# Kernel optimization log

Measured on AMD Instinct MI355X. Metric: run time of the kernel, lower is better.

## Reference

```python
import jax, jax.numpy as jnp
import numpy as np
import itertools

N_OBJECTS = 6  # subsets of range(6), sizes 1..6 -> 63 subsets

def _subset_groups():
    # group subsets by length so each group runs as one batched LSTM
    groups = {}
    for m in range(1, N_OBJECTS + 1):
        for s in itertools.combinations(range(6), m):
            groups.setdefault(m, []).append(list(s))
    return [(m, np.asarray(v, dtype=np.int32)) for m, v in groups.items()]

SUBSET_GROUPS = _subset_groups()


def _lstm_final_h(x, W_ih, W_hh, b_ih, b_hh):
    """x: [B,T,D] -> final hidden state [B,H]. PyTorch gate order i,f,g,o."""
    H = W_hh.shape[1]
    B = x.shape[0]
    # precompute input projections for all timesteps: [B,T,4H]
    xz = jnp.einsum('btd,gd->btg', x, W_ih) + b_ih + b_hh

    def step(carry, xt):
        h, c = carry
        z = xt + h @ W_hh.T
        i, f, g, o = jnp.split(z, 4, axis=-1)
        c = jax.nn.sigmoid(f) * c + jax.nn.sigmoid(i) * jnp.tanh(g)
        h = jax.nn.sigmoid(o) * jnp.tanh(c)
        return (h, c), None

    h0 = jnp.zeros((B, H), x.dtype)
    (h, _), _ = jax.lax.scan(step, (h0, h0), jnp.swapaxes(xz, 0, 1))
    return h


def setup_inputs() -> dict:
    key = jax.random.key(0)
    ks = jax.random.split(key, 10)
    D, H, FC, A = 16, 128, 256, 10
    mb = 8192
    s = lambda k, shape, fan: jax.random.normal(k, shape, jnp.float32) * (1.0 / np.sqrt(fan))
    return {
        'x_input': jax.random.normal(ks[0], (mb, 6, D), jnp.float32),
        'W_ih': s(ks[1], (4 * H, D), D),
        'W_hh': s(ks[2], (4 * H, H), H),
        'b_ih': jnp.zeros((4 * H,), jnp.float32),
        'b_hh': jnp.zeros((4 * H,), jnp.float32),
        'fc1_W': s(ks[3], (FC, H), H),
        'fc1_b': jnp.zeros((FC,), jnp.float32),
        'fc2_W': s(ks[4], (A, FC), FC),
        'fc2_b': jnp.zeros((A,), jnp.float32),
    }


def reference(x_input, W_ih, W_hh, b_ih, b_hh, fc1_W, fc1_b, fc2_W, fc2_b):
    mb = x_input.shape[0]
    H = W_hh.shape[1]
    hs = []
    # subsets of the same length are batched into one LSTM pass (fused form of
    # the original 63-iteration python loop); aggregation is permutation-invariant
    for m, idx in SUBSET_GROUPS:
        nL = idx.shape[0]
        xg = x_input[:, idx, :]                       # [mb, nL, m, D] gather
        xg = xg.reshape(mb * nL, m, x_input.shape[-1])
        h = _lstm_final_h(xg, W_ih, W_hh, b_ih, b_hh)  # [mb*nL, H]
        hs.append(h.reshape(mb, nL, H))
    holder = jnp.concatenate(hs, axis=1)              # [mb, 63, H]
    x = jnp.max(holder, axis=1)                       # aggregate == 'max'
    x = jax.nn.relu(x @ fc1_W.T + fc1_b)
    x = x @ fc2_W.T + fc2_b
    return jax.nn.log_softmax(x, axis=-1)
```

## Files before the change

### kernel.cpp

```cpp
#include <hip/hip_runtime.h>
#include <hip/hip_bf16.h>

#define BLOCK   512
#define NSAMP   16
#define HDIM    128
#define DDIM    16
#define NOBJ    6
#define NNODES  63

typedef __attribute__((ext_vector_type(8))) short bf16x8;
typedef __attribute__((ext_vector_type(4))) float f32x4;

struct Tab { int obj[NNODES]; int depth[NNODES]; };
constexpr void tab_dfs(Tab& t, int& n, int maxel, int depth) {
    for (int j = maxel + 1; j < NOBJ; ++j) {
        t.obj[n] = j; t.depth[n] = depth; ++n;
        tab_dfs(t, n, j, depth + 1);
    }
}
constexpr Tab make_tab() { Tab t{}; int n = 0; tab_dfs(t, n, -1, 1); return t; }
constexpr Tab TAB = make_tab();

#define LOG2E  1.44269504f
#define TWOL2E 2.88539008f

__device__ __forceinline__ float fast_sig(float z, float nb) {
    float e = __builtin_amdgcn_exp2f(fmaf(-LOG2E, z, nb));
    return __builtin_amdgcn_rcpf(1.0f + e);
}
__device__ __forceinline__ float fast_tanh_b(float z, float tb) {
    float e = __builtin_amdgcn_exp2f(fmaf(TWOL2E, z, tb));
    float r = __builtin_amdgcn_rcpf(1.0f + e);
    return fmaf(-2.0f, r, 1.0f);
}
__device__ __forceinline__ float fast_tanh(float y) {
    float e = __builtin_amdgcn_exp2f(y * TWOL2E);
    float r = __builtin_amdgcn_rcpf(1.0f + e);
    return fmaf(-2.0f, r, 1.0f);
}
__device__ __forceinline__ unsigned short f2bf(float x) {
    union { float f; unsigned int u; } a; a.f = x;
    unsigned int r = (a.u + 0x7FFFu + ((a.u >> 16) & 1u)) >> 16;
    return (unsigned short)r;
}


__global__ __launch_bounds__(BLOCK, 2)
void subset_lstm_mfma_kernel(
    const float* __restrict__ x_input,
    const float* __restrict__ W_ih,
    const float* __restrict__ W_hh,
    const float* __restrict__ b_ih,
    const float* __restrict__ b_hh,
    const float* __restrict__ fc1_W,
    const float* __restrict__ fc1_b,
    const float* __restrict__ fc2_W,
    const float* __restrict__ fc2_b,
    float* __restrict__ out)
{
    __shared__ __align__(16) unsigned short hs[5 * 16 * NSAMP * 8];
    __shared__ __align__(16) unsigned short xb[NOBJ * 4 * NSAMP * 8];
    __shared__ float s_maxh[NSAMP * HDIM];
    float* s_fc1   = (float*)hs;
    float* s_logit = (float*)xb;

    const int t      = threadIdx.x;
    const int w      = t >> 6;
    const int lane   = t & 63;
    const int quad   = lane >> 4;
    const int m16    = lane & 15;
    const int s_base = blockIdx.x * NSAMP;

    for (int idx = t; idx < NOBJ * 2 * NSAMP * 8; idx += BLOCK) {
        const int j   = idx & 7;
        const int n   = (idx >> 3) & 15;
        const int q   = (idx >> 7) & 1;
        const int obj = idx >> 8;
        xb[((obj * 4 + q) * NSAMP + n) * 8 + j] =
            f2bf(x_input[(s_base + n) * (NOBJ * DDIM) + obj * DDIM + q * 8 + j]);
        xb[((obj * 4 + 2 + q) * NSAMP + n) * 8 + j] = 0;
    }

    bf16x8 wf[4][5];
    #pragma unroll
    for (int g = 0; g < 4; ++g) {
        const int r = g * HDIM + w * 16 + m16;
        const float* whr = W_hh + r * HDIM;
        const float* wir = W_ih + r * DDIM;
        #pragma unroll
        for (int q = 0; q < 4; ++q) {
            union { unsigned short u[8]; bf16x8 v; } pk;
            #pragma unroll
            for (int j = 0; j < 8; ++j)
                pk.u[j] = f2bf(whr[q * 32 + quad * 8 + j]);
            wf[g][q] = pk.v;
        }
        {
            union { unsigned short u[8]; bf16x8 v; } pk;
            #pragma unroll
            for (int j = 0; j < 8; ++j) {
                float v = 0.0f;
                if (quad == 0) v = wir[j];
                else if (quad == 1) v = wir[8 + j];
                pk.u[j] = f2bf(v);
            }
            wf[g][4] = pk.v;
        }
    }

    float bia[4][4];
    #pragma unroll
    for (int g = 0; g < 4; ++g)
        #pragma unroll
        for (int r = 0; r < 4; ++r) {
            const int c = w * 16 + quad * 4 + r;
            const float b = b_ih[g * HDIM + c] + b_hh[g * HDIM + c];
            bia[g][r] = (g == 2) ? TWOL2E * b : -LOG2E * b;
        }

    float cst[5][4];
    float mh[4] = {-1e30f, -1e30f, -1e30f, -1e30f};

    #pragma unroll
    for (int nd = 0; nd < NNODES; ++nd) {
        const int jo = TAB.obj[nd];
        const int d  = TAB.depth[nd];

        __syncthreads();

        f32x4 acc[4];
        #pragma unroll
        for (int g = 0; g < 4; ++g)
            acc[g] = f32x4{0.f, 0.f, 0.f, 0.f};

        if (d >= 2) {
            const int slot = d - 2;
            #pragma unroll
            for (int q = 0; q < 4; ++q) {
                const bf16x8 bfrag = *(const bf16x8*)
                    &hs[(((slot * 16) + q * 4 + quad) * NSAMP + m16) * 8];
                #pragma unroll
                for (int g = 0; g < 4; ++g)
                    acc[g] = __builtin_amdgcn_mfma_f32_16x16x32_bf16(
                        wf[g][q], bfrag, acc[g], 0, 0, 0);
            }
        }
        {
            const bf16x8 bfrag = *(const bf16x8*)
                &xb[((jo * 4 + quad) * NSAMP + m16) * 8];
            #pragma unroll
            for (int g = 0; g < 4; ++g)
                acc[g] = __builtin_amdgcn_mfma_f32_16x16x32_bf16(
                    wf[g][4], bfrag, acc[g], 0, 0, 0);
        }

        float hn[4];
        #pragma unroll
        for (int r = 0; r < 4; ++r) {
            const float cprev = (d >= 2) ? cst[d - 2][r] : 0.0f;
            const float ig = fast_sig(acc[0][r], bia[0][r]);
            const float fg = fast_sig(acc[1][r], bia[1][r]);
            const float gg = fast_tanh_b(acc[2][r], bia[2][r]);
            const float og = fast_sig(acc[3][r], bia[3][r]);
            const float cn = fmaf(fg, cprev, ig * gg);
            const float h  = og * fast_tanh(cn);
            hn[r] = h;
            mh[r] = fmaxf(mh[r], h);
            if (jo < NOBJ - 1) cst[d - 1][r] = cn;
        }

        if (jo < NOBJ - 1) {
            union { __hip_bfloat162 h2[2]; uint2 v; } hp;
            hp.h2[0] = __float22bfloat162_rn(float2{hn[0], hn[1]});
            hp.h2[1] = __float22bfloat162_rn(float2{hn[2], hn[3]});
            const int kslot = w * 2 + (quad >> 1);
            unsigned short* dst =
                &hs[((((d - 1) * 16) + kslot) * NSAMP + m16) * 8 + (quad & 1) * 4];
            *(uint2*)dst = hp.v;
        }
    }

    __syncthreads();
    #pragma unroll
    for (int r = 0; r < 4; ++r) {
        const int c = w * 16 + quad * 4 + r;
        s_maxh[m16 * HDIM + c] = mh[r];
    }
    __syncthreads();

    {
        const int f  = t & 255;
        const int sh = t >> 8;
        float a1[8];
        #pragma unroll
        for (int s = 0; s < 8; ++s) a1[s] = fc1_b[f];
        for (int k4 = 0; k4 < HDIM / 4; ++k4) {
            const float4 wv = *(const float4*)&fc1_W[f * HDIM + k4 * 4];
            #pragma unroll
            for (int s = 0; s < 8; ++s) {
                const float4 h4 = *(const float4*)&s_maxh[(sh * 8 + s) * HDIM + k4 * 4];
                a1[s] += wv.x * h4.x + wv.y * h4.y + wv.z * h4.z + wv.w * h4.w;
            }
        }
        #pragma unroll
        for (int s = 0; s < 8; ++s)
            s_fc1[(sh * 8 + s) * 256 + f] = fmaxf(a1[s], 0.0f);
    }
    __syncthreads();

    if (t < NSAMP * 10) {
        const int s = t / 10, a = t % 10;
        float acc2 = fc2_b[a];
        for (int f4 = 0; f4 < 256 / 4; ++f4) {
            const float4 wv = *(const float4*)&fc2_W[a * 256 + f4 * 4];
            const float4 v  = *(const float4*)&s_fc1[s * 256 + f4 * 4];
            acc2 += wv.x * v.x + wv.y * v.y + wv.z * v.z + wv.w * v.w;
        }
        s_logit[s * 10 + a] = acc2;
    }
    __syncthreads();

    if (t < NSAMP) {
        float m = -1e30f;
        #pragma unroll
        for (int a = 0; a < 10; ++a) m = fmaxf(m, s_logit[t * 10 + a]);
        float sum = 0.0f;
        #pragma unroll
        for (int a = 0; a < 10; ++a) sum += __expf(s_logit[t * 10 + a] - m);
        const float lse = m + __logf(sum);
        #pragma unroll
        for (int a = 0; a < 10; ++a)
            out[(s_base + t) * 10 + a] = s_logit[t * 10 + a] - lse;
    }
}

extern "C" void kernel_launch(void* const* d_in, const int* in_sizes, int n_in,
                              void* d_out, int out_size, void* d_ws, size_t ws_size,
                              hipStream_t stream)
{
    (void)d_ws; (void)ws_size; (void)n_in; (void)out_size;

    const float* x   = (const float*)d_in[0];
    const float* Wih = (const float*)d_in[1];
    const float* Whh = (const float*)d_in[2];
    const float* bih = (const float*)d_in[3];
    const float* bhh = (const float*)d_in[4];
    const float* f1w = (const float*)d_in[5];
    const float* f1b = (const float*)d_in[6];
    const float* f2w = (const float*)d_in[7];
    const float* f2b = (const float*)d_in[8];

    const int mb = in_sizes[0] / (NOBJ * DDIM);
    dim3 grid(mb / NSAMP), block(BLOCK);
    subset_lstm_mfma_kernel<<<grid, block, 0, stream>>>(
        x, Wih, Whh, bih, bhh, f1w, f1b, f2w, f2b, (float*)d_out);
}
```

Before: 216.4 us.

## Traverse subset tree breadth-first to cut barriers and expose node parallelism

```diff
diff --git a/kernel.cpp b/kernel.cpp
--- a/kernel.cpp
+++ b/kernel.cpp
@@ -6,23 +6,42 @@
 #define HDIM    128
 #define DDIM    16
 #define NOBJ    6
-#define NNODES  63
 
 typedef __attribute__((ext_vector_type(8))) short bf16x8;
 typedef __attribute__((ext_vector_type(4))) float f32x4;
 
-struct Tab { int obj[NNODES]; int depth[NNODES]; };
-constexpr void tab_dfs(Tab& t, int& n, int maxel, int depth) {
-    for (int j = maxel + 1; j < NOBJ; ++j) {
-        t.obj[n] = j; t.depth[n] = depth; ++n;
-        tab_dfs(t, n, j, depth + 1);
-    }
-}
-constexpr Tab make_tab() { Tab t{}; int n = 0; tab_dfs(t, n, -1, 1); return t; }
-constexpr Tab TAB = make_tab();
-
-#define LOG2E  1.44269504f
-#define TWOL2E 2.88539008f
+constexpr int msb6(int m) { int b = -1; for (int i = 0; i < 6; ++i) if (m & (1 << i)) b = i; return b; }
+
+struct BfsTab {
+    int cnt[7];
+    int jo[7][20];
+    int pslot[7][20];
+    int slot[7][20];
+};
+constexpr BfsTab make_bfs() {
+    BfsTab t{};
+    int slotOf[64] = {};
+    for (int d = 1; d <= 6; ++d) {
+        int n = 0, cf = 0;
+        for (int M = 1; M < 64; ++M) {
+            if (__builtin_popcount(M) != d) continue;
+            const int hi = msb6(M);
+            t.jo[d][n] = hi;
+            t.pslot[d][n] = (d == 1) ? -1 : slotOf[M & ~(1 << hi)];
+            if (hi < 5) { t.slot[d][n] = cf; slotOf[M] = cf; ++cf; }
+            else t.slot[d][n] = -1;
+            ++n;
+        }
+        t.cnt[d] = n;
+    }
+    return t;
+}
+constexpr BfsTab BT = make_bfs();
+
+#define LOG2E   1.44269504f
+#define TWOL2E  2.88539008f
+#define SLOT_SZ (16 * NSAMP * 8)
+#define EVEN_OFF (10 * SLOT_SZ)
 
 __device__ __forceinline__ float fast_sig(float z, float nb) {
     float e = __builtin_amdgcn_exp2f(fmaf(-LOG2E, z, nb));
@@ -44,9 +63,8 @@
     return (unsigned short)r;
 }
 
-
 __global__ __launch_bounds__(BLOCK, 2)
-void subset_lstm_mfma_kernel(
+void subset_lstm_bfs_kernel(
     const float* __restrict__ x_input,
     const float* __restrict__ W_ih,
     const float* __restrict__ W_hh,
@@ -58,10 +76,10 @@
     const float* __restrict__ fc2_b,
     float* __restrict__ out)
 {
-    __shared__ __align__(16) unsigned short hs[5 * 16 * NSAMP * 8];
+    __shared__ __align__(16) unsigned short hsbuf[20 * SLOT_SZ];
     __shared__ __align__(16) unsigned short xb[NOBJ * 4 * NSAMP * 8];
-    __shared__ float s_maxh[NSAMP * HDIM];
-    float* s_fc1   = (float*)hs;
+    float* s_maxh  = (float*)(hsbuf + EVEN_OFF);
+    float* s_fc1   = (float*)hsbuf;
     float* s_logit = (float*)xb;
 
     const int t      = threadIdx.x;
@@ -118,65 +136,75 @@
             bia[g][r] = (g == 2) ? TWOL2E * b : -LOG2E * b;
         }
 
-    float cst[5][4];
+    float cA[10][4];
+    float cB[10][4];
     float mh[4] = {-1e30f, -1e30f, -1e30f, -1e30f};
 
     #pragma unroll
-    for (int nd = 0; nd < NNODES; ++nd) {
-        const int jo = TAB.obj[nd];
-        const int d  = TAB.depth[nd];
-
+    for (int d = 1; d <= 6; ++d) {
         __syncthreads();
 
-        f32x4 acc[4];
-        #pragma unroll
-        for (int g = 0; g < 4; ++g)
-            acc[g] = f32x4{0.f, 0.f, 0.f, 0.f};
-
-        if (d >= 2) {
-            const int slot = d - 2;
-            #pragma unroll
-            for (int q = 0; q < 4; ++q) {
+        unsigned short*       curbuf = hsbuf + ((d & 1) ? 0 : EVEN_OFF);
+        const unsigned short* parbuf = hsbuf + (((d - 1) & 1) ? 0 : EVEN_OFF);
+
+        #pragma unroll
+        for (int ni = 0; ni < BT.cnt[d]; ++ni) {
+            const int jo = BT.jo[d][ni];
+            const int ps = BT.pslot[d][ni];
+            const int sl = BT.slot[d][ni];
+
+            f32x4 acc[4];
+            #pragma unroll
+            for (int g = 0; g < 4; ++g)
+                acc[g] = f32x4{0.f, 0.f, 0.f, 0.f};
+
+            if (d >= 2) {
+                #pragma unroll
+                for (int q = 0; q < 4; ++q) {
+                    const bf16x8 bfrag = *(const bf16x8*)
+                        &parbuf[ps * SLOT_SZ + (((q * 4 + quad) * NSAMP) + m16) * 8];
+                    #pragma unroll
+                    for (int g = 0; g < 4; ++g)
+                        acc[g] = __builtin_amdgcn_mfma_f32_16x16x32_bf16(
+                            wf[g][q], bfrag, acc[g], 0, 0, 0);
+                }
+            }
+            {
                 const bf16x8 bfrag = *(const bf16x8*)
-                    &hs[(((slot * 16) + q * 4 + quad) * NSAMP + m16) * 8];
+                    &xb[((jo * 4 + quad) * NSAMP + m16) * 8];
                 #pragma unroll
                 for (int g = 0; g < 4; ++g)
                     acc[g] = __builtin_amdgcn_mfma_f32_16x16x32_bf16(
-                        wf[g][q], bfrag, acc[g], 0, 0, 0);
-            }
-        }
-        {
-            const bf16x8 bfrag = *(const bf16x8*)
-                &xb[((jo * 4 + quad) * NSAMP + m16) * 8];
-            #pragma unroll
-            for (int g = 0; g < 4; ++g)
-                acc[g] = __builtin_amdgcn_mfma_f32_16x16x32_bf16(
-                    wf[g][4], bfrag, acc[g], 0, 0, 0);
-        }
-
-        float hn[4];
-        #pragma unroll
-        for (int r = 0; r < 4; ++r) {
-            const float cprev = (d >= 2) ? cst[d - 2][r] : 0.0f;
-            const float ig = fast_sig(acc[0][r], bia[0][r]);
-            const float fg = fast_sig(acc[1][r], bia[1][r]);
-            const float gg = fast_tanh_b(acc[2][r], bia[2][r]);
-            const float og = fast_sig(acc[3][r], bia[3][r]);
-            const float cn = fmaf(fg, cprev, ig * gg);
-            const float h  = og * fast_tanh(cn);
-            hn[r] = h;
-            mh[r] = fmaxf(mh[r], h);
-            if (jo < NOBJ - 1) cst[d - 1][r] = cn;
-        }
-
-        if (jo < NOBJ - 1) {
-            union { __hip_bfloat162 h2[2]; uint2 v; } hp;
-            hp.h2[0] = __float22bfloat162_rn(float2{hn[0], hn[1]});
-            hp.h2[1] = __float22bfloat162_rn(float2{hn[2], hn[3]});
-            const int kslot = w * 2 + (quad >> 1);
-            unsigned short* dst =
-                &hs[((((d - 1) * 16) + kslot) * NSAMP + m16) * 8 + (quad & 1) * 4];
-            *(uint2*)dst = hp.v;
+                        wf[g][4], bfrag, acc[g], 0, 0, 0);
+            }
+
+            float hn[4];
+            #pragma unroll
+            for (int r = 0; r < 4; ++r) {
+                float cprev = 0.0f;
+                if (d >= 2) cprev = ((d - 1) & 1) ? cA[ps][r] : cB[ps][r];
+                const float ig = fast_sig(acc[0][r], bia[0][r]);
+                const float fg = fast_sig(acc[1][r], bia[1][r]);
+                const float gg = fast_tanh_b(acc[2][r], bia[2][r]);
+                const float og = fast_sig(acc[3][r], bia[3][r]);
+                const float cn = fmaf(fg, cprev, ig * gg);
+                const float h  = og * fast_tanh(cn);
+                hn[r] = h;
+                mh[r] = fmaxf(mh[r], h);
+                if (sl >= 0) {
+                    if (d & 1) cA[sl][r] = cn; else cB[sl][r] = cn;
+                }
+            }
+
+            if (sl >= 0) {
+                union { __hip_bfloat162 h2[2]; uint2 v; } hp;
+                hp.h2[0] = __float22bfloat162_rn(float2{hn[0], hn[1]});
+                hp.h2[1] = __float22bfloat162_rn(float2{hn[2], hn[3]});
+                const int kslot = w * 2 + (quad >> 1);
+                unsigned short* dst =
+                    &curbuf[sl * SLOT_SZ + ((kslot * NSAMP) + m16) * 8 + (quad & 1) * 4];
+                *(uint2*)dst = hp.v;
+            }
         }
     }
 
@@ -252,6 +280,6 @@
 
     const int mb = in_sizes[0] / (NOBJ * DDIM);
     dim3 grid(mb / NSAMP), block(BLOCK);
-    subset_lstm_mfma_kernel<<<grid, block, 0, stream>>>(
+    subset_lstm_bfs_kernel<<<grid, block, 0, stream>>>(
         x, Wih, Whh, bih, bhh, f1w, f1b, f2w, f2b, (float*)d_out);
 }
```

Result: faster. 211.1 us (-2.5%).

## Process subset tree level by level with 16 waves and slot-planned hidden buffers

Applied to the files above, without the earlier changes.

```diff
diff --git a/kernel.cpp b/kernel.cpp
--- a/kernel.cpp
+++ b/kernel.cpp
@@ -1,40 +1,81 @@
 #include <hip/hip_runtime.h>
 #include <hip/hip_bf16.h>
 
-#define BLOCK   512
+#define BLOCK   1024
 #define NSAMP   16
 #define HDIM    128
 #define DDIM    16
 #define NOBJ    6
-#define NNODES  63
+#define NSLOT   16
 
 typedef __attribute__((ext_vector_type(8))) short bf16x8;
 typedef __attribute__((ext_vector_type(4))) float f32x4;
 
-struct Tab { int obj[NNODES]; int depth[NNODES]; };
-constexpr void tab_dfs(Tab& t, int& n, int maxel, int depth) {
-    for (int j = maxel + 1; j < NOBJ; ++j) {
-        t.obj[n] = j; t.depth[n] = depth; ++n;
-        tab_dfs(t, n, j, depth + 1);
-    }
-}
-constexpr Tab make_tab() { Tab t{}; int n = 0; tab_dfs(t, n, -1, 1); return t; }
-constexpr Tab TAB = make_tab();
-
-#define LOG2E  1.44269504f
-#define TWOL2E 2.88539008f
-
-__device__ __forceinline__ float fast_sig(float z, float nb) {
-    float e = __builtin_amdgcn_exp2f(fmaf(-LOG2E, z, nb));
+constexpr int pc6(int m)  { int c = 0; for (int i = 0; i < 6; ++i) c += (m >> i) & 1; return c; }
+constexpr int msb6(int m) { int b = -1; for (int i = 0; i < 6; ++i) if (m & (1 << i)) b = i; return b; }
+
+struct NodeRec { int jo, ps, sl; };
+struct Plan { int cnt[7]; int n1[7]; NodeRec nd[7][20]; };
+constexpr Plan make_plan() {
+    Plan P{};
+    int slotOf[64] = {};
+    bool busy[NSLOT] = {};
+    for (int d = 1; d <= 6; ++d) {
+        int n = 0;
+        for (int M = 1; M < 64; ++M) {
+            if (pc6(M) != d || msb6(M) != 5) continue;
+            P.nd[d][n].jo = 5;
+            P.nd[d][n].ps = (d == 1) ? -1 : slotOf[M & ~(1 << 5)];
+            P.nd[d][n].sl = -1;
+            ++n;
+        }
+        int pend[20] = {}; int np = 0;
+        for (int M = 1; M < 64; ++M) {
+            if (pc6(M) != d || msb6(M) >= 5) continue;
+            const int hi = msb6(M);
+            int fs = -1;
+            for (int s = 0; s < NSLOT; ++s) if (!busy[s]) { fs = s; break; }
+            if (fs >= 0) {
+                busy[fs] = true; slotOf[M] = fs;
+                P.nd[d][n].jo = hi;
+                P.nd[d][n].ps = (d == 1) ? -1 : slotOf[M & ~(1 << hi)];
+                P.nd[d][n].sl = fs;
+                ++n;
+            } else pend[np++] = M;
+        }
+        P.n1[d] = n;
+        int freeds[20] = {}; int nf = 0;
+        if (d >= 2)
+            for (int M = 1; M < 64; ++M)
+                if (pc6(M) == d - 1 && msb6(M) == 4) freeds[nf++] = slotOf[M];
+        for (int i = 0; i < np; ++i) {
+            const int M = pend[i]; const int hi = msb6(M);
+            const int s = freeds[--nf];
+            slotOf[M] = s;
+            P.nd[d][n].jo = hi;
+            P.nd[d][n].ps = slotOf[M & ~(1 << hi)];
+            P.nd[d][n].sl = s;
+            ++n;
+        }
+        P.cnt[d] = n;
+        for (int s = 0; s < NSLOT; ++s) busy[s] = false;
+        for (int M = 1; M < 64; ++M)
+            if (pc6(M) == d && msb6(M) < 5) busy[slotOf[M]] = true;
+    }
+    return P;
+}
+constexpr Plan PL = make_plan();
+
+#define LOG2E   1.44269504f
+#define TWOL2E  2.88539008f
+#define SLOT_SH (16 * NSAMP * 8)
+
+__device__ __forceinline__ float fast_sig(float z) {
+    float e = __builtin_amdgcn_exp2f(-LOG2E * z);
     return __builtin_amdgcn_rcpf(1.0f + e);
 }
-__device__ __forceinline__ float fast_tanh_b(float z, float tb) {
-    float e = __builtin_amdgcn_exp2f(fmaf(TWOL2E, z, tb));
-    float r = __builtin_amdgcn_rcpf(1.0f + e);
-    return fmaf(-2.0f, r, 1.0f);
-}
-__device__ __forceinline__ float fast_tanh(float y) {
-    float e = __builtin_amdgcn_exp2f(y * TWOL2E);
+__device__ __forceinline__ float fast_tanh(float z) {
+    float e = __builtin_amdgcn_exp2f(TWOL2E * z);
     float r = __builtin_amdgcn_rcpf(1.0f + e);
     return fmaf(-2.0f, r, 1.0f);
 }
@@ -45,8 +86,8 @@
 }
 
 
-__global__ __launch_bounds__(BLOCK, 2)
-void subset_lstm_mfma_kernel(
+__global__ __launch_bounds__(BLOCK)
+void subset_lstm_w16_kernel(
     const float* __restrict__ x_input,
     const float* __restrict__ W_ih,
     const float* __restrict__ W_hh,
@@ -58,10 +99,11 @@
     const float* __restrict__ fc2_b,
     float* __restrict__ out)
 {
-    __shared__ __align__(16) unsigned short hs[5 * 16 * NSAMP * 8];
-    __shared__ __align__(16) unsigned short xb[NOBJ * 4 * NSAMP * 8];
-    __shared__ float s_maxh[NSAMP * HDIM];
-    float* s_fc1   = (float*)hs;
+    __shared__ __align__(16) unsigned short hs[NSLOT * SLOT_SH];
+    __shared__ __align__(16) unsigned short xb[NOBJ * 2 * NSAMP * 8];
+    __shared__ __align__(16) unsigned short xpad[16];
+    float* s_maxh  = (float*)hs;
+    float* s_fc1   = (float*)(hs + 4096);
     float* s_logit = (float*)xb;
 
     const int t      = threadIdx.x;
@@ -69,142 +111,128 @@
     const int lane   = t & 63;
     const int quad   = lane >> 4;
     const int m16    = lane & 15;
+    const int cb     = w * 8;
     const int s_base = blockIdx.x * NSAMP;
 
+    if (t < 16) xpad[t] = (t == 0) ? f2bf(1.0f) : (unsigned short)0;
+
     for (int idx = t; idx < NOBJ * 2 * NSAMP * 8; idx += BLOCK) {
-        const int j   = idx & 7;
-        const int n   = (idx >> 3) & 15;
-        const int q   = (idx >> 7) & 1;
-        const int obj = idx >> 8;
-        xb[((obj * 4 + q) * NSAMP + n) * 8 + j] =
-            f2bf(x_input[(s_base + n) * (NOBJ * DDIM) + obj * DDIM + q * 8 + j]);
-        xb[((obj * 4 + 2 + q) * NSAMP + n) * 8 + j] = 0;
-    }
-
-    bf16x8 wf[4][5];
+        const int j = idx & 7, n = (idx >> 3) & 15, q = (idx >> 7) & 1, obj = idx >> 8;
+        xb[idx] = f2bf(x_input[(s_base + n) * (NOBJ * DDIM) + obj * DDIM + q * 8 + j]);
+    }
+
+    bf16x8 wf[2][5];
     #pragma unroll
-    for (int g = 0; g < 4; ++g) {
-        const int r = g * HDIM + w * 16 + m16;
-        const float* whr = W_hh + r * HDIM;
-        const float* wir = W_ih + r * DDIM;
+    for (int T = 0; T < 2; ++T) {
+        const int chan = cb + (m16 >> 1);
+        const int gate = 2 * T + (m16 & 1);
+        const int grow = gate * HDIM + chan;
+        const float* whr = W_hh + grow * HDIM;
+        const float* wir = W_ih + grow * DDIM;
         #pragma unroll
         for (int q = 0; q < 4; ++q) {
             union { unsigned short u[8]; bf16x8 v; } pk;
             #pragma unroll
             for (int j = 0; j < 8; ++j)
                 pk.u[j] = f2bf(whr[q * 32 + quad * 8 + j]);
-            wf[g][q] = pk.v;
+            wf[T][q] = pk.v;
         }
         {
             union { unsigned short u[8]; bf16x8 v; } pk;
             #pragma unroll
             for (int j = 0; j < 8; ++j) {
                 float v = 0.0f;
-                if (quad == 0) v = wir[j];
-                else if (quad == 1) v = wir[8 + j];
+                if (quad < 2) v = wir[quad * 8 + j];
+                else if (quad == 2 && j == 0) v = b_ih[grow] + b_hh[grow];
                 pk.u[j] = f2bf(v);
             }
-            wf[g][4] = pk.v;
-        }
-    }
-
-    float bia[4][4];
+            wf[T][4] = pk.v;
+        }
+    }
+
+    float cs[NSLOT][2];
+    float mh0 = -1e30f, mh1 = -1e30f;
+
     #pragma unroll
-    for (int g = 0; g < 4; ++g)
-        #pragma unroll
-        for (int r = 0; r < 4; ++r) {
-            const int c = w * 16 + quad * 4 + r;
-            const float b = b_ih[g * HDIM + c] + b_hh[g * HDIM + c];
-            bia[g][r] = (g == 2) ? TWOL2E * b : -LOG2E * b;
-        }
-
-    float cst[5][4];
-    float mh[4] = {-1e30f, -1e30f, -1e30f, -1e30f};
-
-    #pragma unroll
-    for (int nd = 0; nd < NNODES; ++nd) {
-        const int jo = TAB.obj[nd];
-        const int d  = TAB.depth[nd];
-
+    for (int d = 1; d <= 6; ++d) {
         __syncthreads();
-
-        f32x4 acc[4];
-        #pragma unroll
-        for (int g = 0; g < 4; ++g)
-            acc[g] = f32x4{0.f, 0.f, 0.f, 0.f};
-
-        if (d >= 2) {
-            const int slot = d - 2;
-            #pragma unroll
-            for (int q = 0; q < 4; ++q) {
-                const bf16x8 bfrag = *(const bf16x8*)
-                    &hs[(((slot * 16) + q * 4 + quad) * NSAMP + m16) * 8];
+        #pragma unroll
+        for (int ni = 0; ni < PL.cnt[d]; ++ni) {
+            if (ni == PL.n1[d]) __syncthreads();
+            const int jo = PL.nd[d][ni].jo;
+            const int ps = PL.nd[d][ni].ps;
+            const int sl = PL.nd[d][ni].sl;
+
+            f32x4 aIF = f32x4{0.f, 0.f, 0.f, 0.f};
+            f32x4 aGO = f32x4{0.f, 0.f, 0.f, 0.f};
+
+            {
+                const unsigned short* bp = (quad < 2)
+                    ? &xb[((jo * 2 + quad) * NSAMP + m16) * 8]
+                    : &xpad[(quad - 2) * 8];
+                const bf16x8 bfx = *(const bf16x8*)bp;
+                aIF = __builtin_amdgcn_mfma_f32_16x16x32_bf16(wf[0][4], bfx, aIF, 0, 0, 0);
+                aGO = __builtin_amdgcn_mfma_f32_16x16x32_bf16(wf[1][4], bfx, aGO, 0, 0, 0);
+            }
+            if (ps >= 0) {
                 #pragma unroll
-                for (int g = 0; g < 4; ++g)
-                    acc[g] = __builtin_amdgcn_mfma_f32_16x16x32_bf16(
-                        wf[g][q], bfrag, acc[g], 0, 0, 0);
-            }
-        }
-        {
-            const bf16x8 bfrag = *(const bf16x8*)
-                &xb[((jo * 4 + quad) * NSAMP + m16) * 8];
-            #pragma unroll
-            for (int g = 0; g < 4; ++g)
-                acc[g] = __builtin_amdgcn_mfma_f32_16x16x32_bf16(
-                    wf[g][4], bfrag, acc[g], 0, 0, 0);
-        }
-
-        float hn[4];
-        #pragma unroll
-        for (int r = 0; r < 4; ++r) {
-            const float cprev = (d >= 2) ? cst[d - 2][r] : 0.0f;
-            const float ig = fast_sig(acc[0][r], bia[0][r]);
-            const float fg = fast_sig(acc[1][r], bia[1][r]);
-            const float gg = fast_tanh_b(acc[2][r], bia[2][r]);
-            const float og = fast_sig(acc[3][r], bia[3][r]);
-            const float cn = fmaf(fg, cprev, ig * gg);
-            const float h  = og * fast_tanh(cn);
-            hn[r] = h;
-            mh[r] = fmaxf(mh[r], h);
-            if (jo < NOBJ - 1) cst[d - 1][r] = cn;
-        }
-
-        if (jo < NOBJ - 1) {
-            union { __hip_bfloat162 h2[2]; uint2 v; } hp;
-            hp.h2[0] = __float22bfloat162_rn(float2{hn[0], hn[1]});
-            hp.h2[1] = __float22bfloat162_rn(float2{hn[2], hn[3]});
-            const int kslot = w * 2 + (quad >> 1);
-            unsigned short* dst =
-                &hs[((((d - 1) * 16) + kslot) * NSAMP + m16) * 8 + (quad & 1) * 4];
-            *(uint2*)dst = hp.v;
-        }
-    }
-
-    __syncthreads();
-    #pragma unroll
-    for (int r = 0; r < 4; ++r) {
-        const int c = w * 16 + quad * 4 + r;
-        s_maxh[m16 * HDIM + c] = mh[r];
+                for (int q = 0; q < 4; ++q) {
+                    const bf16x8 bh = *(const bf16x8*)
+                        &hs[ps * SLOT_SH + (((q * 4 + quad) * NSAMP) + m16) * 8];
+                    aIF = __builtin_amdgcn_mfma_f32_16x16x32_bf16(wf[0][q], bh, aIF, 0, 0, 0);
+                    aGO = __builtin_amdgcn_mfma_f32_16x16x32_bf16(wf[1][q], bh, aGO, 0, 0, 0);
+                }
+            }
+
+            float hnv[2];
+            #pragma unroll
+            for (int u = 0; u < 2; ++u) {
+                const float zi = aIF[2 * u], zf = aIF[2 * u + 1];
+                const float zg = aGO[2 * u], zo = aGO[2 * u + 1];
+                const float cprev = (ps >= 0) ? cs[ps][u] : 0.0f;
+                const float ig = fast_sig(zi);
+                const float fg = fast_sig(zf);
+                const float gg = fast_tanh(zg);
+                const float og = fast_sig(zo);
+                const float cn = fmaf(fg, cprev, ig * gg);
+                const float h  = og * fast_tanh(cn);
+                hnv[u] = h;
+                if (sl >= 0) cs[sl][u] = cn;
+            }
+            mh0 = fmaxf(mh0, hnv[0]);
+            mh1 = fmaxf(mh1, hnv[1]);
+
+            if (sl >= 0) {
+                const __hip_bfloat162 hp = __float22bfloat162_rn(float2{hnv[0], hnv[1]});
+                *(__hip_bfloat162*)&hs[sl * SLOT_SH + ((w * NSAMP) + m16) * 8 + 2 * quad] = hp;
+            }
+        }
+    }
+
+    __syncthreads();
+    {
+        float2 v; v.x = mh0; v.y = mh1;
+        *(float2*)&s_maxh[m16 * HDIM + cb + 2 * quad] = v;
     }
     __syncthreads();
 
     {
         const int f  = t & 255;
         const int sh = t >> 8;
-        float a1[8];
-        #pragma unroll
-        for (int s = 0; s < 8; ++s) a1[s] = fc1_b[f];
+        float a1[4];
+        #pragma unroll
+        for (int s = 0; s < 4; ++s) a1[s] = fc1_b[f];
         for (int k4 = 0; k4 < HDIM / 4; ++k4) {
             const float4 wv = *(const float4*)&fc1_W[f * HDIM + k4 * 4];
             #pragma unroll
-            for (int s = 0; s < 8; ++s) {
-                const float4 h4 = *(const float4*)&s_maxh[(sh * 8 + s) * HDIM + k4 * 4];
+            for (int s = 0; s < 4; ++s) {
+                const float4 h4 = *(const float4*)&s_maxh[(sh * 4 + s) * HDIM + k4 * 4];
                 a1[s] += wv.x * h4.x + wv.y * h4.y + wv.z * h4.z + wv.w * h4.w;
             }
         }
         #pragma unroll
-        for (int s = 0; s < 8; ++s)
-            s_fc1[(sh * 8 + s) * 256 + f] = fmaxf(a1[s], 0.0f);
+        for (int s = 0; s < 4; ++s)
+            s_fc1[(sh * 4 + s) * 256 + f] = fmaxf(a1[s], 0.0f);
     }
     __syncthreads();
 
@@ -252,6 +280,6 @@
 
     const int mb = in_sizes[0] / (NOBJ * DDIM);
     dim3 grid(mb / NSAMP), block(BLOCK);
-    subset_lstm_mfma_kernel<<<grid, block, 0, stream>>>(
+    subset_lstm_w16_kernel<<<grid, block, 0, stream>>>(
         x, Wih, Whh, bih, bhh, f1w, f1b, f2w, f2b, (float*)d_out);
 }
```

Measured after the change: 218.0 us. No clear change (+0.7%).
